# Optimization experiments

Hardware: AMD Instinct MI355X
Metric: run time of the kernel (lower is better)

## Reference

```python
import jax, jax.numpy as jnp
import numpy as np

B, NQ, T, M, DIM, KVD, H, DH = 8, 256, 32, 256, 768, 1024, 8, 64
INNER = H * DH
EPS = 1e-5  # torch LayerNorm default


def _layernorm(z, g, b):
    mu = jnp.mean(z, axis=-1, keepdims=True)
    var = jnp.mean(jnp.square(z - mu), axis=-1, keepdims=True)
    return (z - mu) * jax.lax.rsqrt(var + EPS) * g + b


def setup_inputs() -> dict:
    key = jax.random.key(0)
    ks = jax.random.split(key, 6)
    x = jax.random.normal(ks[0], (B, NQ, DIM), dtype=jnp.float32)
    k_v = jax.random.normal(ks[1], (B, T, M, KVD), dtype=jnp.float32)
    # LayerNorm affine params (torch init: weight=1, bias=0)
    g_q = jnp.ones((DIM,), jnp.float32)
    b_q = jnp.zeros((DIM,), jnp.float32)
    g_kv = jnp.ones((KVD,), jnp.float32)
    b_kv = jnp.zeros((KVD,), jnp.float32)
    # Linear weights (no bias); stored as [in, out] for x @ W
    Wq = jax.random.normal(ks[2], (DIM, INNER), dtype=jnp.float32) * 0.02
    Wkv = jax.random.normal(ks[3], (KVD, 2 * INNER), dtype=jnp.float32) * 0.02
    Wo = jax.random.normal(ks[4], (INNER, DIM), dtype=jnp.float32) * 0.02
    return {"x": x, "k_v": k_v, "g_q": g_q, "b_q": b_q, "g_kv": g_kv,
            "b_kv": b_kv, "Wq": Wq, "Wkv": Wkv, "Wo": Wo}


def reference(x, k_v, g_q, b_q, g_kv, b_kv, Wq, Wkv, Wo):
    scale = DH ** -0.5
    xq = _layernorm(x, g_q, b_q)                       # [b, nq, dim]
    kv = _layernorm(k_v, g_kv, b_kv)                   # [b, t, m, kvd]
    kv = kv.reshape(kv.shape[0], -1, kv.shape[-1])     # [b, tm, kvd]
    q = xq @ Wq                                        # [b, nq, inner]
    kvp = kv @ Wkv                                     # [b, tm, 2*inner]
    k, v = jnp.split(kvp, 2, axis=-1)
    # b n (h d) -> b h n d
    def heads(z):
        return z.reshape(z.shape[0], z.shape[1], H, DH).transpose(0, 2, 1, 3)
    q, k, v = heads(q) * scale, heads(k), heads(v)
    sim = jnp.einsum('bhid,bhjd->bhij', q, k)          # [b, h, nq, tm]
    sim = sim - jax.lax.stop_gradient(jnp.max(sim, axis=-1, keepdims=True))
    attn = jax.nn.softmax(sim, axis=-1)
    out = jnp.einsum('bhij,bhjd->bhid', attn, v)       # [b, h, nq, dh]
    out = out.transpose(0, 2, 1, 3).reshape(out.shape[0], NQ, INNER)
    return out @ Wo                                    # [b, nq, dim]
```

## Files before the change

### kernel.cpp

```cpp
#include <hip/hip_runtime.h>
#include <math.h>

#define NB     8
#define NQX    256
#define TMX    8192
#define DIMX   768
#define KVDX   1024
#define NHX    8
#define DHX    64
#define INNERX 512
#define NSPLIT 8

typedef __bf16 bf16x8 __attribute__((ext_vector_type(8)));
typedef float  f32x4  __attribute__((ext_vector_type(4)));

__device__ inline ushort f2bf(float f) {
    uint u = __float_as_uint(f);
    return (ushort)((u + 0x7FFFu + ((u >> 16) & 1u)) >> 16);
}

template<int COLS>
__global__ __launch_bounds__(256)
void ln_apply_bf16_kernel(const float* __restrict__ in, const float* __restrict__ g,
                          const float* __restrict__ bet, ushort* __restrict__ out)
{
    const int wid  = threadIdx.x >> 6;
    const int lane = threadIdx.x & 63;
    const long row = (long)blockIdx.x * 4 + wid;
    const float4* p4 = (const float4*)(in + row * COLS);
    float4 v[COLS / 256];
    float s = 0.f, ss = 0.f;
#pragma unroll
    for (int c = 0; c < COLS / 256; ++c) {
        v[c] = p4[c * 64 + lane];
        s  += v[c].x + v[c].y + v[c].z + v[c].w;
        ss += v[c].x * v[c].x + v[c].y * v[c].y + v[c].z * v[c].z + v[c].w * v[c].w;
    }
#pragma unroll
    for (int off = 1; off < 64; off <<= 1) {
        s  += __shfl_xor(s,  off, 64);
        ss += __shfl_xor(ss, off, 64);
    }
    const float m  = s * (1.f / COLS);
    const float rs = rsqrtf(ss * (1.f / COLS) - m * m + 1e-5f);
    ushort* orow = out + row * COLS;
#pragma unroll
    for (int c = 0; c < COLS / 256; ++c) {
        float4 gg = ((const float4*)g)[c * 64 + lane];
        float4 bb = ((const float4*)bet)[c * 64 + lane];
        uint2 pk;
        pk.x = f2bf((v[c].x - m) * rs * gg.x + bb.x)
             | ((uint)f2bf((v[c].y - m) * rs * gg.y + bb.y) << 16);
        pk.y = f2bf((v[c].z - m) * rs * gg.z + bb.z)
             | ((uint)f2bf((v[c].w - m) * rs * gg.w + bb.w) << 16);
        *(uint2*)(orow + (c * 64 + lane) * 4) = pk;
    }
}

__global__ __launch_bounds__(256)
void transpose_bf16_kernel(const float* __restrict__ in, ushort* __restrict__ out,
                           int K, int N)
{
    __shared__ float tile[64][65];
    const int t  = threadIdx.x;
    const int n0 = blockIdx.x * 64, k0 = blockIdx.y * 64;
#pragma unroll
    for (int i = 0; i < 16; ++i) {
        int f = i * 256 + t, r = f >> 6, c = f & 63;
        tile[r][c] = in[(size_t)(k0 + r) * N + n0 + c];
    }
    __syncthreads();
#pragma unroll
    for (int i = 0; i < 16; ++i) {
        int f = i * 256 + t, r = f >> 6, c = f & 63;
        out[(size_t)(n0 + r) * K + k0 + c] = f2bf(tile[c][r]);
    }
}

__global__ __launch_bounds__(256)
void gemm_f32_kernel(const float* __restrict__ A, const float* __restrict__ W,
                     float* __restrict__ C, int M, int N, int K)
{
    __shared__ float As[16][132];
    __shared__ float Bs[16][132];
    const int t  = threadIdx.x;
    const int bm = blockIdx.y * 128;
    const int bn = blockIdx.x * 128;
    const int ty = t >> 4, tx = t & 15;
    const int ar = t >> 1, ak0 = (t & 1) * 8;
    const int bk = t >> 4, bn0 = (t & 15) * 8;

    float acc[8][8];
#pragma unroll
    for (int i = 0; i < 8; ++i)
#pragma unroll
        for (int j = 0; j < 8; ++j) acc[i][j] = 0.f;

    const float* Arow = A + (size_t)(bm + ar) * K;

    for (int k0 = 0; k0 < K; k0 += 16) {
        float4 a0 = *(const float4*)(Arow + k0 + ak0);
        float4 a1 = *(const float4*)(Arow + k0 + ak0 + 4);
        const float* Wrow = W + (size_t)(k0 + bk) * N + bn + bn0;
        float4 w0 = *(const float4*)(Wrow);
        float4 w1 = *(const float4*)(Wrow + 4);

        __syncthreads();
        As[ak0 + 0][ar] = a0.x;
        As[ak0 + 1][ar] = a0.y;
        As[ak0 + 2][ar] = a0.z;
        As[ak0 + 3][ar] = a0.w;
        As[ak0 + 4][ar] = a1.x;
        As[ak0 + 5][ar] = a1.y;
        As[ak0 + 6][ar] = a1.z;
        As[ak0 + 7][ar] = a1.w;
        *(float4*)&Bs[bk][bn0]     = w0;
        *(float4*)&Bs[bk][bn0 + 4] = w1;
        __syncthreads();

#pragma unroll
        for (int kk = 0; kk < 16; ++kk) {
            float a[8], b[8];
            *(float4*)&a[0] = *(const float4*)&As[kk][ty * 8];
            *(float4*)&a[4] = *(const float4*)&As[kk][ty * 8 + 4];
            *(float4*)&b[0] = *(const float4*)&Bs[kk][tx * 8];
            *(float4*)&b[4] = *(const float4*)&Bs[kk][tx * 8 + 4];
#pragma unroll
            for (int i = 0; i < 8; ++i)
#pragma unroll
                for (int j = 0; j < 8; ++j)
                    acc[i][j] = fmaf(a[i], b[j], acc[i][j]);
        }
    }

#pragma unroll
    for (int i = 0; i < 8; ++i) {
        float* Crow = C + (size_t)(bm + ty * 8 + i) * N + bn + tx * 8;
        *(float4*)Crow       = make_float4(acc[i][0], acc[i][1], acc[i][2], acc[i][3]);
        *(float4*)(Crow + 4) = make_float4(acc[i][4], acc[i][5], acc[i][6], acc[i][7]);
    }
}

template<bool SWZ>
__global__ __launch_bounds__(256)
void mfma_gemm_bt(const ushort* __restrict__ A, const ushort* __restrict__ Bt,
                  ushort* __restrict__ C, int M, int N, int K, float escale)
{
    __shared__ ushort As[128 * 32];
    __shared__ ushort Bs[128 * 32];
    const int t    = threadIdx.x;
    const int wid  = t >> 6, lane = t & 63;
    const int lr   = lane & 15, quad = lane >> 4;
    const int wq   = wid >> 1, wn = wid & 1;

    int mt_i, nt_i;
    if (SWZ) {
        int flat = blockIdx.x + (int)(gridDim.x * blockIdx.y);
        mt_i = ((flat >> 6) << 3) | (flat & 7);
        nt_i = (flat >> 3) & 7;
    } else {
        mt_i = blockIdx.y; nt_i = blockIdx.x;
    }
    const int bm = mt_i * 128, bn = nt_i * 128;

    f32x4 acc[4][4];
#pragma unroll
    for (int i = 0; i < 4; ++i)
#pragma unroll
        for (int j = 0; j < 4; ++j) acc[i][j] = (f32x4)(0.f);

    for (int k0 = 0; k0 < K; k0 += 32) {
        __syncthreads();
#pragma unroll
        for (int o = 0; o < 2; ++o) {
            int s  = o * 256 + t;
            int n  = s >> 2;
            int kc = (s & 3) ^ ((n >> 2) & 3);
            const ushort* ga = A  + (size_t)(bm + n) * K + k0 + kc * 8;
            const ushort* gb = Bt + (size_t)(bn + n) * K + k0 + kc * 8;
            __builtin_amdgcn_global_load_lds(
                (const __attribute__((address_space(1))) void*)ga,
                (__attribute__((address_space(3))) void*)(&As[0] + o * 2048 + wid * 512),
                16, 0, 0);
            __builtin_amdgcn_global_load_lds(
                (const __attribute__((address_space(1))) void*)gb,
                (__attribute__((address_space(3))) void*)(&Bs[0] + o * 2048 + wid * 512),
                16, 0, 0);
        }
        __syncthreads();

        bf16x8 af[4], bfr[4];
#pragma unroll
        for (int mt = 0; mt < 4; ++mt) {
            int rn = wq * 64 + mt * 16 + lr;
            af[mt] = *(const bf16x8*)&As[rn * 32 + (quad ^ ((rn >> 2) & 3)) * 8];
        }
#pragma unroll
        for (int nt = 0; nt < 4; ++nt) {
            int rn = wn * 64 + nt * 16 + lr;
            bfr[nt] = *(const bf16x8*)&Bs[rn * 32 + (quad ^ ((rn >> 2) & 3)) * 8];
        }
#pragma unroll
        for (int mt = 0; mt < 4; ++mt)
#pragma unroll
            for (int nt = 0; nt < 4; ++nt)
                acc[mt][nt] = __builtin_amdgcn_mfma_f32_16x16x32_bf16(
                    af[mt], bfr[nt], acc[mt][nt], 0, 0, 0);
    }

#pragma unroll
    for (int mt = 0; mt < 4; ++mt)
#pragma unroll
        for (int nt = 0; nt < 4; ++nt) {
            int row = bm + wq * 64 + mt * 16 + quad * 4;
            int col = bn + wn * 64 + nt * 16 + lr;
#pragma unroll
            for (int r = 0; r < 4; ++r)
                C[(size_t)(row + r) * N + col] = f2bf(acc[mt][nt][r] * escale);
        }
}

__global__ __launch_bounds__(512, 2)
void mfma_gemm_bt256(const ushort* __restrict__ A, const ushort* __restrict__ Bt,
                     ushort* __restrict__ C, int M, int N, int K, float escale)
{
    __shared__ __attribute__((aligned(16))) ushort As[4 * 8192];
    __shared__ __attribute__((aligned(16))) ushort Bs[4 * 8192];
    const int t    = threadIdx.x;
    const int wid  = t >> 6, lane = t & 63;
    const int lr   = lane & 15, quad = lane >> 4;
    const int wm   = wid >> 2, wn = wid & 3;

    const int nbn = N >> 8;
    {
    }
    const int nwg = (int)gridDim.x;
    const int swq = nwg >> 3, swr = nwg & 7;
    const int xcd = (int)blockIdx.x & 7, lid = (int)blockIdx.x >> 3;
    const int swzf = (xcd < swr ? xcd * (swq + 1) : swr * (swq + 1) + (xcd - swr) * swq) + lid;
    const int bm = (swzf / nbn) * 256, bn = (swzf % nbn) * 256;

    const int srow = t >> 2;
    const int sseg = (t & 3) ^ ((srow >> 1) & 3);
    const ushort* gA = A  + (size_t)(bm + srow) * K + sseg * 8;
    const ushort* gB = Bt + (size_t)(bn + srow) * K + sseg * 8;
    const size_t rstep = (size_t)128 * K;
    const int ld0 = wid * 512;
    const int ld1 = 4096 + wid * 512;

#define STG256(arr, gp, tt) do {                                               \
        const int _b = (tt) & 3;                                               \
        const ushort* _g = (gp) + (size_t)(tt) * 32;                           \
        __builtin_amdgcn_global_load_lds(                                      \
            (const __attribute__((address_space(1))) void*)_g,                 \
            (__attribute__((address_space(3))) void*)(arr + _b * 8192 + ld0),  \
            16, 0, 0);                                                         \
        __builtin_amdgcn_global_load_lds(                                      \
            (const __attribute__((address_space(1))) void*)(_g + rstep),       \
            (__attribute__((address_space(3))) void*)(arr + _b * 8192 + ld1),  \
            16, 0, 0);                                                         \
    } while (0)

    const int NT = K >> 5;
    STG256(As, gA, 0); STG256(Bs, gB, 0);
    STG256(As, gA, 1); STG256(Bs, gB, 1);
    STG256(As, gA, 2); STG256(Bs, gB, 2);

    f32x4 acc[8][4];
#pragma unroll
    for (int i = 0; i < 8; ++i)
#pragma unroll
        for (int j = 0; j < 4; ++j) acc[i][j] = (f32x4)(0.f);

    const int rseg8 = (quad ^ ((lr >> 1) & 3)) * 8;
    const int aoff = (wm * 128 + lr) * 32 + rseg8;
    const int boff = (wn * 64 + lr) * 32 + rseg8;

    for (int tt = 0; tt < NT; ++tt) {
        const int b = tt & 3;
        if (tt + 2 < NT)      asm volatile("s_waitcnt vmcnt(8)" ::: "memory");
        else if (tt + 1 < NT) asm volatile("s_waitcnt vmcnt(4)" ::: "memory");
        else                  asm volatile("s_waitcnt vmcnt(0)" ::: "memory");
        __builtin_amdgcn_s_barrier();
        asm volatile("" ::: "memory");

        const ushort* Ab = As + b * 8192 + aoff;
        const ushort* Bb = Bs + b * 8192 + boff;

        if (tt + 3 < NT) STG256(As, gA, tt + 3);
        bf16x8 bfr[4], af[4];
#pragma unroll
        for (int n = 0; n < 4; ++n)
            bfr[n] = *(const bf16x8*)(Bb + n * 512);
#pragma unroll
        for (int m = 0; m < 4; ++m)
            af[m] = *(const bf16x8*)(Ab + m * 512);
        __builtin_amdgcn_s_setprio(1);
#pragma unroll
        for (int m = 0; m < 4; ++m)
#pragma unroll
            for (int n = 0; n < 4; ++n)
                acc[m][n] = __builtin_amdgcn_mfma_f32_16x16x32_bf16(
                    af[m], bfr[n], acc[m][n], 0, 0, 0);
        __builtin_amdgcn_s_setprio(0);

        if (tt + 3 < NT) STG256(Bs, gB, tt + 3);
#pragma unroll
        for (int m = 0; m < 4; ++m)
            af[m] = *(const bf16x8*)(Ab + (m + 4) * 512);
        __builtin_amdgcn_s_setprio(1);
#pragma unroll
        for (int m = 0; m < 4; ++m)
#pragma unroll
            for (int n = 0; n < 4; ++n)
                acc[m + 4][n] = __builtin_amdgcn_mfma_f32_16x16x32_bf16(
                    af[m], bfr[n], acc[m + 4][n], 0, 0, 0);
        __builtin_amdgcn_s_setprio(0);
    }
#undef STG256

#pragma unroll
    for (int m = 0; m < 8; ++m)
#pragma unroll
        for (int n = 0; n < 4; ++n) {
            int row = bm + wm * 128 + m * 16 + quad * 4;
            int col = bn + wn * 64 + n * 16 + lr;
#pragma unroll
            for (int r = 0; r < 4; ++r)
                C[(size_t)(row + r) * N + col] = f2bf(acc[m][n][r] * escale);
        }
}

__global__ __launch_bounds__(256)
void attn_mfma_kernel(const ushort* __restrict__ qbuf, const ushort* __restrict__ kvp,
                      float* __restrict__ po, float* __restrict__ pl)
{
    __shared__ ushort Ks[64][72];
    __shared__ ushort Vt[64][72];
    __shared__ ushort Ps[128][72];
    const int t    = threadIdx.x;
    const int w    = t >> 6, lane = t & 63;
    const int lr   = lane & 15, quad = lane >> 4;
    const int qt   = blockIdx.x;
    const int h    = blockIdx.y;
    const int z    = blockIdx.z;
    const int b    = z >> 3, sp = z & 7;

#pragma unroll
    for (int i = 0; i < 4; ++i) {
        int idx = i * 256 + t;
        int row = idx >> 3, c8 = (idx & 7) * 8;
        const ushort* src = qbuf + (size_t)(b * NQX + qt * 128 + row) * INNERX + h * DHX + c8;
        *(uint4*)&Ps[row][c8] = *(const uint4*)src;
    }
    __syncthreads();
    bf16x8 qf[2][2];
#pragma unroll
    for (int mt = 0; mt < 2; ++mt)
#pragma unroll
        for (int ks = 0; ks < 2; ++ks)
            qf[mt][ks] = *(const bf16x8*)&Ps[w * 32 + mt * 16 + lr][ks * 32 + quad * 8];
    __syncthreads();

    f32x4 O[2][4];
    float l_[2][4];
#pragma unroll
    for (int mt = 0; mt < 2; ++mt) {
#pragma unroll
        for (int nt = 0; nt < 4; ++nt) O[mt][nt] = (f32x4)(0.f);
#pragma unroll
        for (int r = 0; r < 4; ++r) l_[mt][r] = 0.f;
    }

    const size_t kvrow0 = (size_t)b * TMX * KVDX + (size_t)(sp * (TMX / NSPLIT)) * KVDX + h * DHX;
    const int vp = t & 31, vdg = t >> 5;

    for (int jt = 0; jt < (TMX / NSPLIT) / 64; ++jt) {
        const ushort* kb = kvp + kvrow0 + (size_t)jt * 64 * KVDX;
        const ushort* kp = kb + (size_t)(t >> 3) * KVDX + (t & 7) * 8;
        uint4 kd0 = *(const uint4*)(kp);
        uint4 kd1 = *(const uint4*)(kp + 32 * KVDX);
        const ushort* vbp = kb + 512 + (size_t)(2 * vp) * KVDX + vdg * 8;
        uint4 vd0 = *(const uint4*)(vbp);
        uint4 vd1 = *(const uint4*)(vbp + KVDX);

        __syncthreads();
        *(uint4*)&Ks[t >> 3][(t & 7) * 8]        = kd0;
        *(uint4*)&Ks[32 + (t >> 3)][(t & 7) * 8] = kd1;
        const uint* v0w = (const uint*)&vd0;
        const uint* v1w = (const uint*)&vd1;
#pragma unroll
        for (int e = 0; e < 8; ++e) {
            uint u0 = (e & 1) ? (v0w[e >> 1] >> 16) : (v0w[e >> 1] & 0xFFFFu);
            uint u1 = (e & 1) ? (v1w[e >> 1] >> 16) : (v1w[e >> 1] & 0xFFFFu);
            *(uint*)&Vt[vdg * 8 + e][2 * vp] = u0 | (u1 << 16);
        }
        __syncthreads();

#pragma unroll
        for (int mt = 0; mt < 2; ++mt) {
            f32x4 s[4];
#pragma unroll
            for (int nt = 0; nt < 4; ++nt) s[nt] = (f32x4)(0.f);
#pragma unroll
            for (int ks = 0; ks < 2; ++ks) {
                bf16x8 kf[4];
#pragma unroll
                for (int nt = 0; nt < 4; ++nt)
                    kf[nt] = *(const bf16x8*)&Ks[nt * 16 + lr][ks * 32 + quad * 8];
#pragma unroll
                for (int nt = 0; nt < 4; ++nt)
                    s[nt] = __builtin_amdgcn_mfma_f32_16x16x32_bf16(
                        qf[mt][ks], kf[nt], s[nt], 0, 0, 0);
            }
#pragma unroll
            for (int r = 0; r < 4; ++r) {
                float p0 = __expf(s[0][r]);
                float p1 = __expf(s[1][r]);
                float p2 = __expf(s[2][r]);
                float p3 = __expf(s[3][r]);
                l_[mt][r] += p0 + p1 + p2 + p3;
                int prow = w * 32 + mt * 16 + quad * 4 + r;
                Ps[prow][lr]      = f2bf(p0);
                Ps[prow][16 + lr] = f2bf(p1);
                Ps[prow][32 + lr] = f2bf(p2);
                Ps[prow][48 + lr] = f2bf(p3);
            }
        }

#pragma unroll
        for (int ks = 0; ks < 2; ++ks) {
            bf16x8 vf[4];
#pragma unroll
            for (int nt = 0; nt < 4; ++nt)
                vf[nt] = *(const bf16x8*)&Vt[nt * 16 + lr][ks * 32 + quad * 8];
#pragma unroll
            for (int mt = 0; mt < 2; ++mt) {
                bf16x8 pf = *(const bf16x8*)&Ps[w * 32 + mt * 16 + lr][ks * 32 + quad * 8];
#pragma unroll
                for (int nt = 0; nt < 4; ++nt)
                    O[mt][nt] = __builtin_amdgcn_mfma_f32_16x16x32_bf16(
                        pf, vf[nt], O[mt][nt], 0, 0, 0);
            }
        }
    }

#pragma unroll
    for (int mt = 0; mt < 2; ++mt)
#pragma unroll
        for (int r = 0; r < 4; ++r) {
            float lv = l_[mt][r];
            lv += __shfl_xor(lv, 1, 64);
            lv += __shfl_xor(lv, 2, 64);
            lv += __shfl_xor(lv, 4, 64);
            lv += __shfl_xor(lv, 8, 64);
            int grow = b * NQX + qt * 128 + w * 32 + mt * 16 + quad * 4 + r;
            float* dst = po + (size_t)(sp * 2048 + grow) * INNERX + h * DHX;
#pragma unroll
            for (int nt = 0; nt < 4; ++nt)
                dst[nt * 16 + lr] = O[mt][nt][r];
            if (lr == 0)
                pl[(sp * 2048 + grow) * NHX + h] = lv;
        }
}

__global__ __launch_bounds__(256)
void combine_kernel(const float* __restrict__ po, const float* __restrict__ pl,
                    float* __restrict__ ao)
{
    int idx = blockIdx.x * 256 + threadIdx.x;
    int row = idx >> 7;
    int col = (idx & 127) * 4;
    int h   = col >> 6;
    float L = 0.f;
#pragma unroll
    for (int s = 0; s < NSPLIT; ++s)
        L += pl[(s * 2048 + row) * NHX + h];
    float rL = 1.f / L;
    float4 r = make_float4(0.f, 0.f, 0.f, 0.f);
#pragma unroll
    for (int s = 0; s < NSPLIT; ++s) {
        float4 a = *(const float4*)(po + (size_t)(s * 2048 + row) * INNERX + col);
        r.x += a.x; r.y += a.y; r.z += a.z; r.w += a.w;
    }
    r.x *= rL; r.y *= rL; r.z *= rL; r.w *= rL;
    *(float4*)(ao + (size_t)row * INNERX + col) = r;
}

extern "C" void kernel_launch(void* const* d_in, const int* in_sizes, int n_in,
                              void* d_out, int out_size, void* d_ws, size_t ws_size,
                              hipStream_t stream)
{
    (void)in_sizes; (void)n_in; (void)out_size; (void)ws_size;
    const float* x    = (const float*)d_in[0];
    const float* k_v  = (const float*)d_in[1];
    const float* g_q  = (const float*)d_in[2];
    const float* b_q  = (const float*)d_in[3];
    const float* g_kv = (const float*)d_in[4];
    const float* b_kv = (const float*)d_in[5];
    const float* Wq   = (const float*)d_in[6];
    const float* Wkv  = (const float*)d_in[7];
    const float* Wo   = (const float*)d_in[8];
    float* out = (float*)d_out;

    float* ws       = (float*)d_ws;
    float*  pl      = ws;
    ushort* qbuf    = (ushort*)(ws + 131072);
    float*  ao      = ws + 131072;
    ushort* Wkvt    = (ushort*)(ws + 1179648);
    ushort* xln     = (ushort*)(ws + 1703936);
    ushort* Wqt     = (ushort*)(ws + 1703936 + 786432);
    ushort* kvln    = (ushort*)(ws + 1703936);
    float*  po      = ws + 1703936;
    ushort* kvp     = (ushort*)(ws + 35258368);

    ln_apply_bf16_kernel<DIMX><<<(NB * NQX) / 4, 256, 0, stream>>>(x, g_q, b_q, xln);
    transpose_bf16_kernel<<<dim3(INNERX / 64, DIMX / 64), 256, 0, stream>>>(
        Wq, Wqt, DIMX, INNERX);
    mfma_gemm_bt<false><<<dim3(INNERX / 128, (NB * NQX) / 128), 256, 0, stream>>>(
        xln, Wqt, qbuf, NB * NQX, INNERX, DIMX, 0.125f);

    ln_apply_bf16_kernel<KVDX><<<(NB * TMX) / 4, 256, 0, stream>>>(k_v, g_kv, b_kv, kvln);
    transpose_bf16_kernel<<<dim3((2 * INNERX) / 64, KVDX / 64), 256, 0, stream>>>(
        Wkv, Wkvt, KVDX, 2 * INNERX);
    mfma_gemm_bt256<<<dim3((NB * TMX / 256) * ((2 * INNERX) / 256)), 512, 0, stream>>>(
        kvln, Wkvt, kvp, NB * TMX, 2 * INNERX, KVDX, 1.f);

    attn_mfma_kernel<<<dim3(NQX / 128, NHX, NB * NSPLIT), 256, 0, stream>>>(
        qbuf, kvp, po, pl);

    combine_kernel<<<1024, 256, 0, stream>>>(po, pl, ao);
    gemm_f32_kernel<<<dim3(DIMX / 128, (NB * NQX) / 128), 256, 0, stream>>>(
        ao, Wo, out, NB * NQX, DIMX, INNERX);
}
```

Before: 730.4 us.

## Double-buffer LDS fragments in 256-tile GEMM to overlap reads with MFMA

Result: no change. 727.9 us (-0.3%).

```diff
diff --git a/kernel.cpp b/kernel.cpp
--- a/kernel.cpp
+++ b/kernel.cpp
@@ -232,8 +232,6 @@
     const int wm   = wid >> 2, wn = wid & 3;
 
     const int nbn = N >> 8;
-    {
-    }
     const int nwg = (int)gridDim.x;
     const int swq = nwg >> 3, swr = nwg & 7;
     const int xcd = (int)blockIdx.x & 7, lid = (int)blockIdx.x >> 3;
@@ -276,47 +274,52 @@
     const int aoff = (wm * 128 + lr) * 32 + rseg8;
     const int boff = (wn * 64 + lr) * 32 + rseg8;
 
-    for (int tt = 0; tt < NT; ++tt) {
-        const int b = tt & 3;
-        if (tt + 2 < NT)      asm volatile("s_waitcnt vmcnt(8)" ::: "memory");
-        else if (tt + 1 < NT) asm volatile("s_waitcnt vmcnt(4)" ::: "memory");
-        else                  asm volatile("s_waitcnt vmcnt(0)" ::: "memory");
-        __builtin_amdgcn_s_barrier();
-        asm volatile("" ::: "memory");
-
-        const ushort* Ab = As + b * 8192 + aoff;
-        const ushort* Bb = Bs + b * 8192 + boff;
-
-        if (tt + 3 < NT) STG256(As, gA, tt + 3);
-        bf16x8 bfr[4], af[4];
-#pragma unroll
-        for (int n = 0; n < 4; ++n)
-            bfr[n] = *(const bf16x8*)(Bb + n * 512);
-#pragma unroll
-        for (int m = 0; m < 4; ++m)
-            af[m] = *(const bf16x8*)(Ab + m * 512);
-        __builtin_amdgcn_s_setprio(1);
-#pragma unroll
-        for (int m = 0; m < 4; ++m)
-#pragma unroll
-            for (int n = 0; n < 4; ++n)
-                acc[m][n] = __builtin_amdgcn_mfma_f32_16x16x32_bf16(
-                    af[m], bfr[n], acc[m][n], 0, 0, 0);
-        __builtin_amdgcn_s_setprio(0);
-
-        if (tt + 3 < NT) STG256(Bs, gB, tt + 3);
-#pragma unroll
-        for (int m = 0; m < 4; ++m)
-            af[m] = *(const bf16x8*)(Ab + (m + 4) * 512);
-        __builtin_amdgcn_s_setprio(1);
-#pragma unroll
-        for (int m = 0; m < 4; ++m)
-#pragma unroll
-            for (int n = 0; n < 4; ++n)
-                acc[m + 4][n] = __builtin_amdgcn_mfma_f32_16x16x32_bf16(
-                    af[m], bfr[n], acc[m + 4][n], 0, 0, 0);
-        __builtin_amdgcn_s_setprio(0);
-    }
+    bf16x8 ax[8], bx[4], ay[8], by[4];
+
+    asm volatile("s_waitcnt vmcnt(8)" ::: "memory");
+    __builtin_amdgcn_s_barrier();
+    asm volatile("" ::: "memory");
+    {
+        const ushort* Ab = As + aoff;
+        const ushort* Bb = Bs + boff;
+#pragma unroll
+        for (int n = 0; n < 4; ++n) bx[n] = *(const bf16x8*)(Bb + n * 512);
+#pragma unroll
+        for (int m = 0; m < 8; ++m) ax[m] = *(const bf16x8*)(Ab + m * 512);
+    }
+
+#define PROC(t_, CA, CB, NA, NBR) do {                                         \
+        if ((t_) + 1 < NT) {                                                   \
+            if ((t_) + 2 < NT) asm volatile("s_waitcnt vmcnt(4)" ::: "memory");\
+            else               asm volatile("s_waitcnt vmcnt(0)" ::: "memory");\
+            __builtin_amdgcn_s_barrier();                                      \
+            asm volatile("" ::: "memory");                                     \
+            const ushort* Ab_ = As + (((t_) + 1) & 3) * 8192 + aoff;           \
+            const ushort* Bb_ = Bs + (((t_) + 1) & 3) * 8192 + boff;           \
+            _Pragma("unroll")                                                  \
+            for (int n = 0; n < 4; ++n) NBR[n] = *(const bf16x8*)(Bb_ + n * 512);\
+            _Pragma("unroll")                                                  \
+            for (int m = 0; m < 4; ++m) NA[m] = *(const bf16x8*)(Ab_ + m * 512);\
+            if ((t_) + 3 < NT) STG256(As, gA, (t_) + 3);                       \
+            _Pragma("unroll")                                                  \
+            for (int m = 4; m < 8; ++m) NA[m] = *(const bf16x8*)(Ab_ + m * 512);\
+            if ((t_) + 3 < NT) STG256(Bs, gB, (t_) + 3);                       \
+        }                                                                      \
+        __builtin_amdgcn_s_setprio(1);                                         \
+        _Pragma("unroll")                                                      \
+        for (int m = 0; m < 8; ++m)                                            \
+            _Pragma("unroll")                                                  \
+            for (int n = 0; n < 4; ++n)                                        \
+                acc[m][n] = __builtin_amdgcn_mfma_f32_16x16x32_bf16(           \
+                    CA[m], CB[n], acc[m][n], 0, 0, 0);                         \
+        __builtin_amdgcn_s_setprio(0);                                         \
+    } while (0)
+
+    for (int tt = 0; tt < NT; tt += 2) {
+        PROC(tt,     ax, bx, ay, by);
+        PROC(tt + 1, ay, by, ax, bx);
+    }
+#undef PROC
 #undef STG256
 
 #pragma unroll
```
